# Kernel optimization log

Measured on AMD Instinct MI355X. Metric: run time of the kernel, lower is better.

The kernel has to match this reference:

```python
import jax, jax.numpy as jnp
import numpy as np

B, C_IN, T, H, W = 32, 1024, 7, 14, 14
C_INTER = 512


def setup_inputs() -> dict:
    key = jax.random.key(0)
    ks = jax.random.split(key, 8)
    s = lambda fan_in: 1.0 / np.sqrt(fan_in)
    return {
        "x_window": jax.random.normal(ks[0], (B, C_IN, T, H, W), jnp.float32),
        "nodes": jax.random.normal(ks[1], (T, C_INTER), jnp.float32),
        "Wq": jax.random.normal(ks[2], (C_IN, C_INTER), jnp.float32) * s(C_IN),
        "bq": jnp.zeros((C_INTER,), jnp.float32),
        "Wk": jax.random.normal(ks[3], (C_INTER, C_INTER), jnp.float32) * s(C_INTER),
        "bk": jnp.zeros((C_INTER,), jnp.float32),
        "Wv": jax.random.normal(ks[4], (C_IN, C_INTER), jnp.float32) * s(C_IN),
        "bv": jnp.zeros((C_INTER,), jnp.float32),
        "Wo": jax.random.normal(ks[5], (C_INTER, C_IN), jnp.float32) * s(C_INTER),
        "bo": jnp.zeros((C_IN,), jnp.float32),
    }


def reference(x_window, nodes, Wq, bq, Wk, bk, Wv, bv, Wo, bo):
    # x_window: (B, C_in, T, H, W); dropout is identity at eval time.
    t_mid = x_window.shape[2] // 2
    x_item = x_window[:, :, t_mid]                                   # (B, C_in, H, W)
    # pointwise (Linear3d) projections over channel dim
    query = jnp.einsum("bchw,cd->bdhw", x_item, Wq) + bq[None, :, None, None]
    key = nodes @ Wk + bk                                            # (T, C_inter)
    value = jnp.einsum("bcthw,cd->bdthw", x_window, Wv) + bv[None, :, None, None, None]
    # per-pixel attention scores over the T node keys
    alpha = jnp.einsum("bdhw,td->bthw", query, key)                  # (B, T, H, W)
    alpha = jax.nn.softmax(alpha, axis=1)
    # per-pixel weighted temporal sum
    y = jnp.einsum("bthw,bdthw->bdhw", alpha, value)                 # (B, C_inter, H, W)
    out = jnp.einsum("bdhw,dc->bchw", y, Wo) + bo[None, :, None, None]
    return out[:, :, None]                                           # (B, C_in, 1, H, W)
```

## Files before the change

### kernel.cpp

```cpp
#include <hip/hip_runtime.h>
#include <hip/hip_bf16.h>
#include <hip/hip_cooperative_groups.h>
#include <stdint.h>

namespace cg = cooperative_groups;

#define BB    32
#define CIN   1024
#define TT    7
#define HHWW  196
#define HW4   49
#define CI    512
#define TMID  3
#define MM    (BB*HHWW)
#define NCH   32
#define CSZ   32
#define GRID  512
#define NPROD 256

using bf16 = __hip_bfloat16;
typedef __attribute__((ext_vector_type(8))) short short8;
typedef __attribute__((ext_vector_type(4))) short s16x4;
typedef __attribute__((ext_vector_type(4))) float f32x4;

__device__ __forceinline__ void gload_lds16(const void* g, void* l) {
    __builtin_amdgcn_global_load_lds((const __attribute__((address_space(1))) void*)g,
                                     (__attribute__((address_space(3))) void*)l, 16, 0, 0);
}

__device__ __forceinline__ void ctr_inc(int* p) {
    __hip_atomic_fetch_add(p, 1, __ATOMIC_RELEASE, __HIP_MEMORY_SCOPE_AGENT);
}
__device__ __forceinline__ void ctr_wait(int* p, int tgt) {
    while (__hip_atomic_load(p, __ATOMIC_ACQUIRE, __HIP_MEMORY_SCOPE_AGENT) < tgt)
        __builtin_amdgcn_s_sleep(8);
}

template <int EPI>
__device__ __forceinline__ void gemm_body(const bf16* __restrict__ A, const bf16* __restrict__ Bt,
                                          void* __restrict__ Cout, const float* __restrict__ bias,
                                          int M, int N, int K, int bm, int bn,
                                          bf16* As, bf16* Bs) {
    int tid = threadIdx.x;
    int wid = tid >> 6, lane = tid & 63;
    int wr = wid >> 1, wc = wid & 1;
    f32x4 acc[4][4] = {};
    const bf16* Ab = A + (size_t)bm * 128 * K;
    const bf16* Bb = Bt + (size_t)bn * 128 * K;
    int row = lane & 15;
    int kb_base = (lane >> 4) * 8;

    for (int k0 = 0; k0 < K; k0 += 64) {
        #pragma unroll
        for (int it = 0; it < 4; ++it) {
            int e = (it * 256 + tid) * 8;
            int r = e >> 6, cc = e & 63;
            gload_lds16(Ab + (size_t)r * K + k0 + cc, &As[e]);
            gload_lds16(Bb + (size_t)r * K + k0 + cc, &Bs[e]);
        }
        __syncthreads();
        #pragma unroll
        for (int kk = 0; kk < 2; ++kk) {
            int kb = kk * 32 + kb_base;
            short8 a[4], b[4];
            #pragma unroll
            for (int mi = 0; mi < 4; ++mi) a[mi] = *(const short8*)&As[(wr * 64 + mi * 16 + row) * 64 + kb];
            #pragma unroll
            for (int ni = 0; ni < 4; ++ni) b[ni] = *(const short8*)&Bs[(wc * 64 + ni * 16 + row) * 64 + kb];
            #pragma unroll
            for (int mi = 0; mi < 4; ++mi)
                #pragma unroll
                for (int ni = 0; ni < 4; ++ni)
                    acc[mi][ni] = __builtin_amdgcn_mfma_f32_16x16x32_bf16(a[mi], b[ni], acc[mi][ni], 0, 0, 0);
        }
        __syncthreads();
    }

    int col_l = lane & 15, row_l = (lane >> 4) * 4;
    if constexpr (EPI == 0) {
        bf16* C = (bf16*)Cout;
        #pragma unroll
        for (int mi = 0; mi < 4; ++mi) {
            int row0 = bm * 128 + wr * 64 + mi * 16 + row_l;
            #pragma unroll
            for (int ni = 0; ni < 4; ++ni) {
                int col = bn * 128 + wc * 64 + ni * 16 + col_l;
                #pragma unroll
                for (int r = 0; r < 4; ++r)
                    C[(size_t)(row0 + r) * N + col] = __float2bfloat16(acc[mi][ni][r]);
            }
        }
    } else {
        float* Cf = (float*)Cout;
        #pragma unroll
        for (int ni = 0; ni < 4; ++ni) {
            int n = bn * 128 + wc * 64 + ni * 16 + col_l;
            float bz = bias[n];
            #pragma unroll
            for (int mi = 0; mi < 4; ++mi) {
                int m0 = bm * 128 + wr * 64 + mi * 16 + row_l;
                int b = m0 / HHWW;
                int hw0 = m0 - b * HHWW;
                f32x4 v = acc[mi][ni];
                v[0] += bz; v[1] += bz; v[2] += bz; v[3] += bz;
                *(f32x4*)&Cf[((size_t)b * CIN + n) * HHWW + hw0] = v;
            }
        }
    }
}

__device__ __forceinline__ void phase_prep1_unit(
    int u, int tid, float* sred,
    const float* __restrict__ nodes, const float* __restrict__ Wk, const float* __restrict__ bk,
    float* __restrict__ key,
    const float* __restrict__ Wv, const float* __restrict__ Wo,
    bf16* __restrict__ Wv_bf, bf16* __restrict__ WoT_bf,
    const float* __restrict__ bv, const float* __restrict__ bo, float* __restrict__ bvo) {
    if (u < 56) {
        int t = u >> 3, dc = u & 7;
        int d_l = tid & 63, q = tid >> 6;
        int d = dc * 64 + d_l;
        float acc = 0.f;
        const float* nr = nodes + t * CI;
        #pragma unroll 4
        for (int c = q * 128; c < q * 128 + 128; ++c)
            acc = fmaf(nr[c], Wk[(size_t)c * CI + d], acc);
        sred[q * 64 + d_l] = acc;
        __syncthreads();
        if (q == 0)
            key[t * CI + d] = sred[d_l] + sred[64 + d_l] + sred[128 + d_l] + sred[192 + d_l] + bk[d];
    } else if (u < 56 + 2048) {
        int i = (u - 56) * 256 + tid;
        Wv_bf[i] = __float2bfloat16(Wv[i]);
        int d = i >> 10, cp = i & 1023;
        WoT_bf[(size_t)cp * CI + d] = __float2bfloat16(Wo[i]);
    } else {
        int cp0 = (u - 2104) * 32;
        int cp_l = tid & 31, dq = tid >> 5;
        float acc = 0.f;
        #pragma unroll 4
        for (int d = dq * 64; d < dq * 64 + 64; ++d)
            acc = fmaf(bv[d], Wo[(size_t)d * CIN + cp0 + cp_l], acc);
        sred[dq * 32 + cp_l] = acc;
        __syncthreads();
        if (dq == 0) {
            float v = bo[cp0 + cp_l];
            #pragma unroll
            for (int g = 0; g < 8; ++g) v += sred[g * 32 + cp_l];
            bvo[cp0 + cp_l] = v;
        }
    }
}

__device__ __forceinline__ void phase_wqk_unit(
    int cbase, int tid,
    const float* __restrict__ Wq, const float* __restrict__ bq,
    const float* __restrict__ key, float* __restrict__ Wqk, float* __restrict__ bqk) {
    int c = cbase + (tid >> 6);
    int lane = tid & 63;
    if (c > CIN) return;
    const float* src = (c < CIN) ? (Wq + (size_t)c * CI) : bq;
    float acc[TT] = {};
    #pragma unroll 2
    for (int it = 0; it < CI / 64; ++it) {
        float w = src[it * 64 + lane];
        #pragma unroll
        for (int t = 0; t < TT; ++t) acc[t] = fmaf(w, key[t * CI + it * 64 + lane], acc[t]);
    }
    #pragma unroll
    for (int t = 0; t < TT; ++t) {
        float v = acc[t];
        for (int off = 32; off; off >>= 1) v += __shfl_down(v, off);
        if (lane == 0) { if (c < CIN) Wqk[c * 8 + t] = v; else bqk[t] = v; }
    }
}

__device__ __forceinline__ void phase_alpha_unit(
    int ch, int b, int tid, float* wq_s,
    const float* __restrict__ x, const float* __restrict__ Wqk, float* __restrict__ part) {
    for (int i = tid; i < CSZ * 8; i += 256) wq_s[i] = Wqk[ch * CSZ * 8 + i];
    __syncthreads();
    if (tid < HHWW) {
        float acc[TT] = {};
        const float* xb = x + (size_t)(b * CIN + ch * CSZ) * TT * HHWW + TMID * HHWW + tid;
        #pragma unroll 8
        for (int c = 0; c < CSZ; ++c) {
            float v = xb[(size_t)c * TT * HHWW];
            #pragma unroll
            for (int t = 0; t < TT; ++t) acc[t] = fmaf(v, wq_s[c * 8 + t], acc[t]);
        }
        #pragma unroll
        for (int t = 0; t < TT; ++t)
            part[((size_t)(b * NCH + ch) * TT + t) * HHWW + tid] = acc[t];
    }
}

__device__ __forceinline__ void phase_softmax_unit(
    int b, int tid,
    const float* __restrict__ part, const float* __restrict__ bqk, float* __restrict__ alphaF) {
    if (tid >= HHWW) return;
    float s[TT];
    #pragma unroll
    for (int t = 0; t < TT; ++t) s[t] = bqk[t];
    for (int ch = 0; ch < NCH; ++ch)
        #pragma unroll
        for (int t = 0; t < TT; ++t)
            s[t] += part[((size_t)(b * NCH + ch) * TT + t) * HHWW + tid];
    float mx = s[0];
    #pragma unroll
    for (int t = 1; t < TT; ++t) mx = fmaxf(mx, s[t]);
    float e[TT], sum = 0.f;
    #pragma unroll
    for (int t = 0; t < TT; ++t) { e[t] = __expf(s[t] - mx); sum += e[t]; }
    float inv = 1.f / sum;
    #pragma unroll
    for (int t = 0; t < TT; ++t) alphaF[(size_t)b * TT * HHWW + t * HHWW + tid] = e[t] * inv;
}

__device__ __forceinline__ void phase_smxw_unit(
    int c0, int b, int tid, float* al, bf16* txp,
    const float* __restrict__ x, const float* __restrict__ alphaF, bf16* __restrict__ xw) {
    for (int i = tid; i < TT * HHWW; i += 256) al[i] = alphaF[(size_t)b * TT * HHWW + i];
    __syncthreads();
    const f32x4* xp = (const f32x4*)x;
    f32x4 acc[7] = {};
    #pragma unroll
    for (int t = 0; t < TT; ++t) {
        #pragma unroll
        for (int k = 0; k < 7; ++k) {
            int w = k * 256 + tid;
            if (k == 6 && w >= 1568) continue;
            int c_l = w / 49;
            int hw4 = w - c_l * 49;
            f32x4 a4 = *(const f32x4*)&al[t * HHWW + hw4 * 4];
            f32x4 xv = xp[((size_t)(b * CIN + c0 + c_l) * TT + t) * HW4 + hw4];
            acc[k] += a4 * xv;
        }
    }
    #pragma unroll
    for (int k = 0; k < 7; ++k) {
        int w = k * 256 + tid;
        if (k == 6 && w >= 1568) continue;
        int c_l = w / 49;
        int hw4 = w - c_l * 49;
        int v = (hw4 & 7) << 2;
        #pragma unroll
        for (int r = 0; r < 4; ++r)
            txp[(hw4 * 4 + r) * 32 + (c_l ^ v)] = __float2bfloat16(acc[k][r]);
    }
    __syncthreads();
    #pragma unroll
    for (int k = 0; k < 7; ++k) {
        int w = k * 256 + tid;
        if (k == 6 && w >= 1568) continue;
        int m = w >> 3, seg = w & 7;
        int v = ((m >> 2) & 7) << 2;
        s16x4 val = *(const s16x4*)&txp[m * 32 + ((seg * 4) ^ v)];
        *(s16x4*)&xw[(size_t)(b * HHWW + m) * CIN + c0 + seg * 4] = val;
    }
}

__global__ __launch_bounds__(256, 2) void mega(
    const float* __restrict__ x, const float* __restrict__ nodes,
    const float* __restrict__ Wq, const float* __restrict__ bq,
    const float* __restrict__ Wk, const float* __restrict__ bk,
    const float* __restrict__ Wv, const float* __restrict__ bv,
    const float* __restrict__ Wo, const float* __restrict__ bo,
    float* __restrict__ key, float* __restrict__ Wqk, float* __restrict__ bqk,
    float* __restrict__ bvo, bf16* __restrict__ Wv_bf, bf16* __restrict__ WoT_bf,
    bf16* __restrict__ WvoT, float* __restrict__ part, float* __restrict__ alphaF,
    bf16* __restrict__ xw, float* __restrict__ out, int* ctr) {

    cg::grid_group grid = cg::this_grid();
    __shared__ __align__(16) char smem[32768];
    bf16* As = (bf16*)smem;
    bf16* Bs = (bf16*)(smem + 16384);
    int gid = blockIdx.x, tid = threadIdx.x;

    if (gid == 0 && tid < 97) ctr[tid] = 0;
    for (int u = gid; u < 2136; u += GRID) {
        __syncthreads();
        phase_prep1_unit(u, tid, (float*)smem, nodes, Wk, bk, key, Wv, Wo, Wv_bf, WoT_bf, bv, bo, bvo);
    }
    grid.sync();

    if (gid < 257) phase_wqk_unit(gid * 4, tid, Wq, bq, key, Wqk, bqk);
    grid.sync();

    #pragma unroll 1
    for (int r = 0; r < 2; ++r) {
        int u = gid + r * GRID;
        __syncthreads();
        phase_alpha_unit(u & (NCH - 1), u >> 5, tid, (float*)smem, x, Wqk, part);
        __syncthreads();
        if (tid == 0) { __threadfence(); ctr_inc(&ctr[u >> 5]); }
    }

    if (gid >= NPROD) {
        if (gid < NPROD + 32) {
            int b = gid - NPROD;
            if (tid == 0) ctr_wait(&ctr[b], NCH);
            __syncthreads();
            phase_softmax_unit(b, tid, part, bqk, alphaF);
            __syncthreads();
            if (tid == 0) { __threadfence(); ctr_inc(&ctr[32 + b]); }
        }
        int pid = gid - NPROD;
        #pragma unroll 1
        for (int r = 0; r < 4; ++r) {
            int u = pid + r * NPROD;
            int b = u >> 5, c0 = (u & 31) * 32;
            if (tid == 0) ctr_wait(&ctr[32 + b], 1);
            __syncthreads();
            phase_smxw_unit(c0, b, tid, (float*)smem, (bf16*)(smem + 5504), x, alphaF, xw);
            __syncthreads();
            if (tid == 0) { __threadfence(); ctr_inc(&ctr[64 + b]); }
        }
    } else {
        if (gid < 64) {
            gemm_body<0>(WoT_bf, Wv_bf, (void*)WvoT, nullptr, 1024, 1024, 512, gid >> 3, gid & 7, As, Bs);
            __syncthreads();
            if (tid == 0) { __threadfence(); ctr_inc(&ctr[96]); }
        }
        #pragma unroll 1
        for (int t = gid; t < 392; t += NPROD) {
            int bm = t >> 3, bn = t & 7;
            int b0 = (bm * 128) / HHWW, b1 = (bm * 128 + 127) / HHWW;
            if (tid == 0) {
                ctr_wait(&ctr[64 + b0], 32);
                ctr_wait(&ctr[64 + b1], 32);
                ctr_wait(&ctr[96], 64);
            }
            __syncthreads();
            gemm_body<1>(xw, WvoT, (void*)out, bvo, MM, CIN, CIN, bm, bn, As, Bs);
            __syncthreads();
        }
    }
}

__global__ __launch_bounds__(256) void k_prep1(
    const float* __restrict__ nodes, const float* __restrict__ Wk, const float* __restrict__ bk,
    float* __restrict__ key, const float* __restrict__ Wv, const float* __restrict__ Wo,
    bf16* __restrict__ Wv_bf, bf16* __restrict__ WoT_bf,
    const float* __restrict__ bv, const float* __restrict__ bo, float* __restrict__ bvo) {
    __shared__ float sred[256];
    phase_prep1_unit(blockIdx.x, threadIdx.x, sred, nodes, Wk, bk, key, Wv, Wo, Wv_bf, WoT_bf, bv, bo, bvo);
}

__global__ __launch_bounds__(256) void k_prep2(
    const bf16* __restrict__ WoT_bf, const bf16* __restrict__ Wv_bf, bf16* __restrict__ WvoT,
    const float* __restrict__ Wq, const float* __restrict__ bq,
    const float* __restrict__ key, float* __restrict__ Wqk, float* __restrict__ bqk) {
    __shared__ __align__(16) bf16 As[128 * 64];
    __shared__ __align__(16) bf16 Bs[128 * 64];
    int bid = blockIdx.x;
    if (bid < 64) gemm_body<0>(WoT_bf, Wv_bf, (void*)WvoT, nullptr, 1024, 1024, 512, bid >> 3, bid & 7, As, Bs);
    else phase_wqk_unit((bid - 64) * 4, threadIdx.x, Wq, bq, key, Wqk, bqk);
}

__global__ __launch_bounds__(256) void k_alpha(const float* __restrict__ x,
                                               const float* __restrict__ Wqk,
                                               float* __restrict__ part) {
    __shared__ float wq_s[CSZ * 8];
    phase_alpha_unit(blockIdx.x, blockIdx.y, threadIdx.x, wq_s, x, Wqk, part);
}

__global__ __launch_bounds__(256) void k_softmaxF(const float* __restrict__ part,
                                                  const float* __restrict__ bqk,
                                                  float* __restrict__ alphaF) {
    phase_softmax_unit(blockIdx.x, threadIdx.x, part, bqk, alphaF);
}

__global__ __launch_bounds__(256) void k_smxw(const float* __restrict__ x,
                                              const float* __restrict__ alphaF,
                                              bf16* __restrict__ xw) {
    __shared__ __align__(16) float al[TT * HHWW];
    __shared__ __align__(16) bf16 txp[HHWW * 32];
    phase_smxw_unit(blockIdx.x * 32, blockIdx.y, threadIdx.x, al, txp, x, alphaF, xw);
}

__global__ __launch_bounds__(256) void k_gemm1(const bf16* __restrict__ A, const bf16* __restrict__ Bt,
                                               float* __restrict__ C, const float* __restrict__ bias) {
    __shared__ __align__(16) bf16 As[128 * 64];
    __shared__ __align__(16) bf16 Bs[128 * 64];
    gemm_body<1>(A, Bt, (void*)C, bias, MM, CIN, CIN, blockIdx.x, blockIdx.y, As, Bs);
}

extern "C" void kernel_launch(void* const* d_in, const int* in_sizes, int n_in,
                              void* d_out, int out_size, void* d_ws, size_t ws_size,
                              hipStream_t stream) {
    const float* x     = (const float*)d_in[0];
    const float* nodes = (const float*)d_in[1];
    const float* Wq    = (const float*)d_in[2];
    const float* bq    = (const float*)d_in[3];
    const float* Wk    = (const float*)d_in[4];
    const float* bk    = (const float*)d_in[5];
    const float* Wv    = (const float*)d_in[6];
    const float* bv    = (const float*)d_in[7];
    const float* Wo    = (const float*)d_in[8];
    const float* bo    = (const float*)d_in[9];

    uint8_t* w = (uint8_t*)d_ws;
    size_t off = 0;
    auto alloc = [&](size_t bytes) -> void* {
        void* p = w + off;
        off = (off + bytes + 255) & ~(size_t)255;
        return p;
    };
    float* key    = (float*)alloc((size_t)TT * CI * 4);
    float* Wqk    = (float*)alloc((size_t)CIN * 8 * 4);
    float* bqk    = (float*)alloc(8 * 4);
    float* bvo    = (float*)alloc((size_t)CIN * 4);
    bf16*  Wv_bf  = (bf16*)alloc((size_t)CIN * CI * 2);
    bf16*  WoT_bf = (bf16*)alloc((size_t)CIN * CI * 2);
    bf16*  WvoT   = (bf16*)alloc((size_t)CIN * CIN * 2);
    float* part   = (float*)alloc((size_t)BB * NCH * TT * HHWW * 4);
    float* alphaF = (float*)alloc((size_t)BB * TT * HHWW * 4);
    bf16*  xw     = (bf16*)alloc((size_t)MM * CIN * 2);
    int*   ctr    = (int*)alloc(128 * 4);
    float* outp   = (float*)d_out;
    (void)ws_size;

    bool use_coop = false;
    int dev = 0;
    if (hipGetDevice(&dev) == hipSuccess) {
        int coop = 0, ncu = 0, nb = 0;
        hipDeviceGetAttribute(&coop, hipDeviceAttributeCooperativeLaunch, dev);
        hipDeviceGetAttribute(&ncu, hipDeviceAttributeMultiprocessorCount, dev);
        if (coop == 1 &&
            hipOccupancyMaxActiveBlocksPerMultiprocessor(&nb, (const void*)mega, 256, 0) == hipSuccess &&
            nb * ncu >= GRID) {
            use_coop = true;
        }
    }

    if (use_coop) {
        void* kargs[] = {
            (void*)&x, (void*)&nodes, (void*)&Wq, (void*)&bq, (void*)&Wk, (void*)&bk,
            (void*)&Wv, (void*)&bv, (void*)&Wo, (void*)&bo,
            (void*)&key, (void*)&Wqk, (void*)&bqk, (void*)&bvo,
            (void*)&Wv_bf, (void*)&WoT_bf, (void*)&WvoT, (void*)&part, (void*)&alphaF,
            (void*)&xw, (void*)&outp, (void*)&ctr
        };
        if (hipLaunchCooperativeKernel((const void*)mega, dim3(GRID), dim3(256), kargs, 0, stream)
            == hipSuccess)
            return;
    }

    k_prep1<<<2136, 256, 0, stream>>>(nodes, Wk, bk, key, Wv, Wo, Wv_bf, WoT_bf, bv, bo, bvo);
    k_prep2<<<321, 256, 0, stream>>>(WoT_bf, Wv_bf, WvoT, Wq, bq, key, Wqk, bqk);
    k_alpha<<<dim3(NCH, BB), 256, 0, stream>>>(x, Wqk, part);
    k_softmaxF<<<BB, 256, 0, stream>>>(part, bqk, alphaF);
    k_smxw<<<dim3(32, BB), 256, 0, stream>>>(x, alphaF, xw);
    k_gemm1<<<dim3(49, 8), 256, 0, stream>>>(xw, WvoT, (float*)d_out, bvo);
}
```

Baseline: 103.7 us.

## Replace grid sync with counters and fuse softmax into last alpha chunk

Removes the second grid-wide barrier. The Wqk phase now signals a counter, and blocks 448-511 compute the WvoT weight GEMM at the same time as Wqk. Alpha chunks grow from 32 to 64 channels, so there are half as many units, and the last block to finish a batch runs that batch's softmax, detected with an acq_rel atomic. Smxw work is spread over all 512 blocks, and the final GEMM gets one tile per block. The aim is to cut barrier stalls and idle producer/consumer splits, at the cost of more reliance on spin-wait ordering and the co-residency of all blocks.

```diff
diff --git a/kernel.cpp b/kernel.cpp
--- a/kernel.cpp
+++ b/kernel.cpp
@@ -13,10 +13,9 @@
 #define CI    512
 #define TMID  3
 #define MM    (BB*HHWW)
-#define NCH   32
-#define CSZ   32
+#define NCH   16
+#define CSZ   64
 #define GRID  512
-#define NPROD 256
 
 using bf16 = __hip_bfloat16;
 typedef __attribute__((ext_vector_type(8))) short short8;
@@ -30,6 +29,9 @@
 
 __device__ __forceinline__ void ctr_inc(int* p) {
     __hip_atomic_fetch_add(p, 1, __ATOMIC_RELEASE, __HIP_MEMORY_SCOPE_AGENT);
+}
+__device__ __forceinline__ int ctr_inc_acqrel(int* p) {
+    return __hip_atomic_fetch_add(p, 1, __ATOMIC_ACQ_REL, __HIP_MEMORY_SCOPE_AGENT);
 }
 __device__ __forceinline__ void ctr_wait(int* p, int tgt) {
     while (__hip_atomic_load(p, __ATOMIC_ACQUIRE, __HIP_MEMORY_SCOPE_AGENT) < tgt)
@@ -273,68 +275,70 @@
 
     cg::grid_group grid = cg::this_grid();
     __shared__ __align__(16) char smem[32768];
+    __shared__ int sflag;
     bf16* As = (bf16*)smem;
     bf16* Bs = (bf16*)(smem + 16384);
     int gid = blockIdx.x, tid = threadIdx.x;
 
-    if (gid == 0 && tid < 97) ctr[tid] = 0;
+    if (gid == 0 && tid < 128) ctr[tid] = 0;
     for (int u = gid; u < 2136; u += GRID) {
         __syncthreads();
         phase_prep1_unit(u, tid, (float*)smem, nodes, Wk, bk, key, Wv, Wo, Wv_bf, WoT_bf, bv, bo, bvo);
     }
     grid.sync();
 
-    if (gid < 257) phase_wqk_unit(gid * 4, tid, Wq, bq, key, Wqk, bqk);
-    grid.sync();
+    if (gid < 257) {
+        phase_wqk_unit(gid * 4, tid, Wq, bq, key, Wqk, bqk);
+        __syncthreads();
+        if (tid == 0) { __threadfence(); ctr_inc(&ctr[97]); }
+    } else if (gid >= 448) {
+        int t0 = gid - 448;
+        gemm_body<0>(WoT_bf, Wv_bf, (void*)WvoT, nullptr, 1024, 1024, 512, t0 >> 3, t0 & 7, As, Bs);
+        __syncthreads();
+        if (tid == 0) { __threadfence(); ctr_inc(&ctr[96]); }
+    }
+
+    if (gid < 448) {
+        if (tid == 0) ctr_wait(&ctr[97], 257);
+        __syncthreads();
+        int nu = (gid < 64) ? 2 : 1;
+        for (int r = 0; r < nu; ++r) {
+            int u = (r == 0) ? gid : (448 + gid);
+            int b = u >> 4, ch = u & 15;
+            __syncthreads();
+            phase_alpha_unit(ch, b, tid, (float*)smem, x, Wqk, part);
+            __syncthreads();
+            if (tid == 0) sflag = (ctr_inc_acqrel(&ctr[b]) == NCH - 1);
+            __syncthreads();
+            if (sflag) {
+                phase_softmax_unit(b, tid, part, bqk, alphaF);
+                __syncthreads();
+                if (tid == 0) { __threadfence(); ctr_inc(&ctr[32 + b]); }
+            }
+        }
+    }
 
     #pragma unroll 1
     for (int r = 0; r < 2; ++r) {
         int u = gid + r * GRID;
-        __syncthreads();
-        phase_alpha_unit(u & (NCH - 1), u >> 5, tid, (float*)smem, x, Wqk, part);
-        __syncthreads();
-        if (tid == 0) { __threadfence(); ctr_inc(&ctr[u >> 5]); }
-    }
-
-    if (gid >= NPROD) {
-        if (gid < NPROD + 32) {
-            int b = gid - NPROD;
-            if (tid == 0) ctr_wait(&ctr[b], NCH);
-            __syncthreads();
-            phase_softmax_unit(b, tid, part, bqk, alphaF);
-            __syncthreads();
-            if (tid == 0) { __threadfence(); ctr_inc(&ctr[32 + b]); }
-        }
-        int pid = gid - NPROD;
-        #pragma unroll 1
-        for (int r = 0; r < 4; ++r) {
-            int u = pid + r * NPROD;
-            int b = u >> 5, c0 = (u & 31) * 32;
-            if (tid == 0) ctr_wait(&ctr[32 + b], 1);
-            __syncthreads();
-            phase_smxw_unit(c0, b, tid, (float*)smem, (bf16*)(smem + 5504), x, alphaF, xw);
-            __syncthreads();
-            if (tid == 0) { __threadfence(); ctr_inc(&ctr[64 + b]); }
-        }
-    } else {
-        if (gid < 64) {
-            gemm_body<0>(WoT_bf, Wv_bf, (void*)WvoT, nullptr, 1024, 1024, 512, gid >> 3, gid & 7, As, Bs);
-            __syncthreads();
-            if (tid == 0) { __threadfence(); ctr_inc(&ctr[96]); }
-        }
-        #pragma unroll 1
-        for (int t = gid; t < 392; t += NPROD) {
-            int bm = t >> 3, bn = t & 7;
-            int b0 = (bm * 128) / HHWW, b1 = (bm * 128 + 127) / HHWW;
-            if (tid == 0) {
-                ctr_wait(&ctr[64 + b0], 32);
-                ctr_wait(&ctr[64 + b1], 32);
-                ctr_wait(&ctr[96], 64);
-            }
-            __syncthreads();
-            gemm_body<1>(xw, WvoT, (void*)out, bvo, MM, CIN, CIN, bm, bn, As, Bs);
-            __syncthreads();
-        }
+        int b = u >> 5, c0 = (u & 31) * 32;
+        if (tid == 0) ctr_wait(&ctr[32 + b], 1);
+        __syncthreads();
+        phase_smxw_unit(c0, b, tid, (float*)smem, (bf16*)(smem + 5504), x, alphaF, xw);
+        __syncthreads();
+        if (tid == 0) { __threadfence(); ctr_inc(&ctr[64 + b]); }
+    }
+
+    if (gid < 392) {
+        int bm = gid >> 3, bn = gid & 7;
+        int b0 = (bm * 128) / HHWW, b1 = (bm * 128 + 127) / HHWW;
+        if (tid == 0) {
+            ctr_wait(&ctr[96], 64);
+            ctr_wait(&ctr[64 + b0], 32);
+            ctr_wait(&ctr[64 + b1], 32);
+        }
+        __syncthreads();
+        gemm_body<1>(xw, WvoT, (void*)out, bvo, MM, CIN, CIN, bm, bn, As, Bs);
     }
 }
 
```

After: 102.0 us. No clear change (-1.6%).
